# Kernel optimization log

Measured on AMD Instinct MI355X. Metric: run time of the kernel, lower is better.

The kernel has to match this reference:

```python
import jax, jax.numpy as jnp
import numpy as np

TOPK = 2


def _conv2d(x, w, b):
    # x: (B, Cin, H, W), w: (Cout, Cin, 3, 3), SAME padding (padding=1)
    y = jax.lax.conv_general_dilated(
        x, w, window_strides=(1, 1), padding='SAME',
        dimension_numbers=('NCHW', 'OIHW', 'NCHW'))
    return y + b[None, :, None, None]


def _msunit(x2d, c1w, c1b, c2w, c2b):
    # TimesNet-style 2D unit: conv(1->d_model) -> GELU -> conv(d_model->1)
    h = jax.nn.gelu(_conv2d(x2d, c1w, c1b))
    return _conv2d(h, c2w, c2b)


def setup_inputs():
    B, T, H, DM = 256, 2048, 720, 64
    key = jax.random.key(0)
    ks = jax.random.split(key, 5)
    x = jax.random.normal(ks[0], (B, 1, T), jnp.float32)
    conv1_w = jax.random.normal(ks[1], (DM, 1, 3, 3), jnp.float32) * 0.1
    conv1_b = jnp.zeros((DM,), jnp.float32)
    conv2_w = jax.random.normal(ks[2], (1, DM, 3, 3), jnp.float32) * 0.1
    conv2_b = jnp.zeros((1,), jnp.float32)
    head_w = jax.random.normal(ks[3], (H, T), jnp.float32) * 0.02
    head_b = jnp.zeros((H,), jnp.float32)
    return {'x': x, 'conv1_w': conv1_w, 'conv1_b': conv1_b,
            'conv2_w': conv2_w, 'conv2_b': conv2_b,
            'head_w': head_w, 'head_b': head_b}


def reference(x, conv1_w, conv1_b, conv2_w, conv2_b, head_w, head_b):
    B, _, T = x.shape
    # FFT amplitude spectrum, batch-averaged, drop DC bin
    amp = jnp.abs(jnp.fft.rfft(x[:, 0, :], axis=-1)).mean(0)[1:]
    vals, idx = jax.lax.top_k(amp, TOPK)
    # data-dependent period selection (mirrors .item() calls in torch -> Python ints)
    freqs = np.asarray(idx) + 1
    P_list = [max(1, int(round(T / int(f)))) for f in freqs]
    weights = jax.nn.softmax(vals.astype(x.dtype))
    y = jnp.zeros_like(x)
    for i, P in enumerate(P_list):
        cols = (T + P - 1) // P
        pad = P * cols - T
        xp = jnp.pad(x, ((0, 0), (0, 0), (0, pad)))
        x2d = xp.reshape(B, 1, cols, P).transpose(0, 1, 3, 2)  # (B,1,P,cols)
        y2d = _msunit(x2d, conv1_w, conv1_b, conv2_w, conv2_b)  # (B,1,P,cols)
        y1d = y2d.transpose(0, 1, 3, 2).reshape(B, 1, cols * P)[..., :T]
        y = y + weights[i] * y1d
    out = y[:, 0, :] @ head_w.T + head_b  # (B, horizon)
    return out
```

## Files before the change

### kernel.cpp

```cpp
#include <hip/hip_runtime.h>
#include <hip/hip_fp16.h>
#include <math.h>

#define T_LEN   2048
#define NB      256
#define N_FREQ  1024
#define DMODEL  64
#define HORIZON 720

#define WS_AMP  64
#define WS_Y0   2048
#define WS_Y1   (2048 + NB * T_LEN)

#define PMAX_FAST 191
#define CHUNK   1024
#define NCHUNK  2
#define HSTRIDE 1412
#define ZSLOT   1408
#define XS2N    1796
#define ZXS     1795

typedef _Float16 h4 __attribute__((ext_vector_type(4)));
typedef float    fx4 __attribute__((ext_vector_type(4)));

__device__ __forceinline__ float gelu_fast(float a) {
    float a2 = a * a;
    float z  = a * fmaf(-0.07135481627159498f, a2, -1.5957691216057308f);
    float e  = __expf(z);
    return a * __builtin_amdgcn_rcpf(1.0f + e);
}

__device__ __forceinline__ __half2 gelu2(float x, float y) {
    __half2 a  = __float22half2_rn(make_float2(x, y));
    __half2 a2 = __hmul2(a, a);
    const __half2 c2 = __float2half2_rn(-0.07135481627159498f);
    const __half2 c1 = __float2half2_rn(-1.5957691216057308f);
    __half2 z = __hmul2(a, __hfma2(c2, a2, c1));
    __half2 e = h2exp(z);
    const __half2 one = __float2half2_rn(1.0f);
    return __hmul2(a, h2rcp(__hadd2(one, e)));
}

__device__ __forceinline__ h4 gelu4(fx4 h) {
    union { __half2 p[2]; h4 v; } u;
    u.p[0] = gelu2(h[0], h[1]);
    u.p[1] = gelu2(h[2], h[3]);
    return u.v;
}

__device__ __forceinline__ float2 cmul(float2 a, float2 b) {
    return make_float2(a.x * b.x - a.y * b.y, a.x * b.y + a.y * b.x);
}

__device__ __forceinline__ unsigned magic_div(unsigned d) {
    return (unsigned)((0x100000000ULL + d - 1) / d);
}

__device__ __forceinline__ void compute_meta(const float* __restrict__ amp,
                                             float* sf, int* si, int tid,
                                             int& P1, int& cols1, int& P2, int& cols2,
                                             float& wg1, float& wg2) {
    float* v1s = sf;        float* v2s = sf + 256;
    int*   i1s = si;        int*   i2s = si + 256;
    float4 v4 = ((const float4*)amp)[tid];
    float vv[4] = {v4.x, v4.y, v4.z, v4.w};
    float v1 = -1e30f, v2 = -1e30f; int i1 = 1 << 30, i2 = 1 << 30;
    #pragma unroll
    for (int u = 0; u < 4; ++u) {
        int j = tid * 4 + u;
        float v = vv[u];
        if (v > v1) { v2 = v1; i2 = i1; v1 = v; i1 = j; }
        else if (v > v2) { v2 = v; i2 = j; }
    }
    v1s[tid] = v1; i1s[tid] = i1; v2s[tid] = v2; i2s[tid] = i2;
    __syncthreads();
    for (int st = 128; st > 0; st >>= 1) {
        if (tid < st) {
            float w1 = v1s[tid + st]; int j1 = i1s[tid + st];
            float w2 = v2s[tid + st]; int j2 = i2s[tid + st];
            float a1 = v1s[tid];      int a1i = i1s[tid];
            float a2 = v2s[tid];      int a2i = i2s[tid];
            float n1, n2; int n1i, n2i;
            bool w1_first = (w1 > a1) || (w1 == a1 && j1 < a1i);
            if (w1_first) {
                n1 = w1; n1i = j1;
                bool a1_next = (a1 > w2) || (a1 == w2 && a1i < j2);
                if (a1_next) { n2 = a1; n2i = a1i; } else { n2 = w2; n2i = j2; }
            } else {
                n1 = a1; n1i = a1i;
                bool w1_next = (w1 > a2) || (w1 == a2 && j1 < a2i);
                if (w1_next) { n2 = w1; n2i = j1; } else { n2 = a2; n2i = a2i; }
            }
            v1s[tid] = n1; i1s[tid] = n1i; v2s[tid] = n2; i2s[tid] = n2i;
        }
        __syncthreads();
    }
    float v1f = v1s[0], v2f = v2s[0];
    int f1 = i1s[0] + 1, f2 = i2s[0] + 1;
    __syncthreads();
    P1 = (int)llround(2048.0 / (double)f1); if (P1 < 1) P1 = 1;
    P2 = (int)llround(2048.0 / (double)f2); if (P2 < 1) P2 = 1;
    cols1 = (T_LEN + P1 - 1) / P1;
    cols2 = (T_LEN + P2 - 1) / P2;
    float mx = fmaxf(v1f, v2f);
    float e1 = __expf(v1f - mx), e2 = __expf(v2f - mx);
    float inv = 1.0f / (e1 + e2);
    wg1 = e1 * inv; wg2 = e2 * inv;
}

__global__ __launch_bounds__(256) void fft_amp_kernel(const float* __restrict__ x,
                                                      float* __restrict__ amp,
                                                      float* __restrict__ out) {
    __shared__ float2 buf0[1024];
    __shared__ float2 buf1[1024];
    __shared__ float2 tw[512];
    const int tid = threadIdx.x;
    const int b = blockIdx.x;

    if (tid < 180) {
        const int zi = b * 180 + tid;
        ((float4*)out)[zi] = make_float4(0.f, 0.f, 0.f, 0.f);
    }

    {
        float s, c;
        __sincosf((float)tid * 6.135923151542565e-3f, &s, &c);
        tw[tid] = make_float2(c, -s);
        __sincosf((float)(tid + 256) * 6.135923151542565e-3f, &s, &c);
        tw[tid + 256] = make_float2(c, -s);
    }
    const float2* xz = (const float2*)(x + b * T_LEN);
    buf0[tid]       = xz[tid];
    buf0[tid + 256] = xz[tid + 256];
    buf0[tid + 512] = xz[tid + 512];
    buf0[tid + 768] = xz[tid + 768];
    __syncthreads();

    float2* src = buf0;
    float2* dst = buf1;
    for (int s = 0; s < 10; s += 2) {
        const int Ns = 1 << s;
        const int j1 = tid;
        const int q  = j1 & (Ns - 1);
        const int hi = j1 >> s;
        float2 A = src[j1];
        float2 B = src[j1 + 512];
        float2 C = src[j1 + 256];
        float2 D = src[j1 + 768];
        float2 w  = tw[q << (9 - s)];
        float2 wB = cmul(w, B);
        float2 wD = cmul(w, D);
        float2 P0 = make_float2(A.x + wB.x, A.y + wB.y);
        float2 P1 = make_float2(A.x - wB.x, A.y - wB.y);
        float2 Q0 = make_float2(C.x + wD.x, C.y + wD.y);
        float2 Q1 = make_float2(C.x - wD.x, C.y - wD.y);
        float2 wa = tw[q << (8 - s)];
        float2 wb = tw[(q + Ns) << (8 - s)];
        float2 t0 = cmul(wa, Q0);
        float2 t1 = cmul(wb, Q1);
        const int O = (hi << (s + 2)) + q;
        dst[O]          = make_float2(P0.x + t0.x, P0.y + t0.y);
        dst[O + 2 * Ns] = make_float2(P0.x - t0.x, P0.y - t0.y);
        dst[O + Ns]     = make_float2(P1.x + t1.x, P1.y + t1.y);
        dst[O + 3 * Ns] = make_float2(P1.x - t1.x, P1.y - t1.y);
        __syncthreads();
        float2* tmp = src; src = dst; dst = tmp;
    }
    const int rot = (b * 8) & 1023;
    #pragma unroll
    for (int j = 0; j < 4; ++j) {
        const int kk = (tid + j * 256 + rot) & 1023;
        const int k  = kk + 1;
        float mag;
        if (k == 1024) {
            float2 Z0 = src[0];
            mag = fabsf(Z0.x - Z0.y) * (1.0f / 256.0f);
        } else {
            float2 Zk = src[k];
            float2 Zn = src[1024 - k];
            float Ax = 0.5f * (Zk.x + Zn.x), Ay = 0.5f * (Zk.y - Zn.y);
            float Bx = 0.5f * (Zk.y + Zn.y), By = -0.5f * (Zk.x - Zn.x);
            float sn, cs;
            __sincosf((float)k * 3.0679615757712823e-3f, &sn, &cs);
            float Xx = Ax + cs * Bx + sn * By;
            float Xy = Ay + cs * By - sn * Bx;
            mag = sqrtf(Xx * Xx + Xy * Xy) * (1.0f / 256.0f);
        }
        atomicAdd(amp + kk, mag);
    }
}

__global__ __launch_bounds__(256) void conv_fast_kernel(
    const float* __restrict__ x,
    const float* __restrict__ w1, const float* __restrict__ b1,
    const float* __restrict__ w2, const float* __restrict__ b2,
    const float* __restrict__ amp,
    float* __restrict__ ws)
{
    __shared__ __align__(16) _Float16 xs2[XS2N];
    __shared__ __align__(16) _Float16 dk[9][HSTRIDE];

    const int tid = threadIdx.x;
    const int b   = blockIdx.x >> 1;
    const int ci  = blockIdx.x & 1;
    const int t0  = ci * CHUNK;
    const int bT  = b * T_LEN;

    for (int j = tid; j < XS2N; j += 256) {
        const int t = t0 - 384 + j;
        xs2[j] = (_Float16)((j < 1792 && t >= 0 && t < T_LEN) ? x[bT + t] : 0.f);
    }

    int P1, cols1, P2, cols2; float wg1, wg2;
    compute_meta(amp, (float*)dk, (int*)dk + 512, tid, P1, cols1, P2, cols2, wg1, wg2);

    if (blockIdx.x == 0 && blockIdx.y == 0 && tid == 0) {
        int* mi = (int*)ws;
        mi[0] = P1; mi[1] = cols1; mi[2] = P2; mi[3] = cols2;
        ws[4] = wg1; ws[5] = wg2;
    }

    const int per  = blockIdx.y;
    const int P    = per == 0 ? P1 : P2;
    const int cols = per == 0 ? cols1 : cols2;
    if (P > PMAX_FAST || P < 2) return;
    const float wgt = per == 0 ? wg1 : wg2;
    float* yout = ws + (per == 0 ? WS_Y0 : WS_Y1);

    const int U0  = t0 - (P + 1);
    const int HN  = CHUNK + 2 * P + 2;
    const unsigned MP = magic_div((unsigned)P);
    const int IB0 = 383 - P;

    const int lane = tid & 63;
    const int wv   = tid >> 6;
    const int lm   = lane & 15;
    const int lg   = lane >> 4;

    h4  w1f[4], w2f[4];
    fx4 b1f[4];
    #pragma unroll
    for (int t = 0; t < 4; ++t) {
        #pragma unroll
        for (int i = 0; i < 4; ++i) {
            const int k = lg * 4 + i;
            w1f[t][i] = (_Float16)((k < 9) ? w1[(t * 16 + lm) * 9 + k] : 0.f);
            w2f[t][i] = (_Float16)((lm < 9) ? w2[(t * 16 + k) * 9 + lm] : 0.f);
            b1f[t][i] = b1[t * 16 + k];
        }
    }

    const int HN16 = (HN + 15) >> 4;
    const fx4 zf4 = {0.f, 0.f, 0.f, 0.f};

    for (int nt = wv; nt < HN16; nt += 4) {
        const int ih = nt * 16 + lm;
        const int u  = U0 + ih;
        const int uu = u < 0 ? 0 : u;
        const int cc = (int)__umulhi((unsigned)uu, MP);
        const int pp = uu - cc * P;
        const bool rm = pp > 0, rp = pp < P - 1, cm = cc > 0, cp = (cc + 1) < cols;
        const int ibase = ih + IB0;
        h4 xb;
        #pragma unroll
        for (int j = 0; j < 4; ++j) {
            const int tap = lg * 4 + j;
            const int q = (tap * 86) >> 8;
            const int r = tap - q * 3;
            const bool ok = (tap < 9)
                && (q > 0 || rm) && (q < 2 || rp)
                && (r > 0 || cm) && (r < 2 || cp);
            const int addr = ok ? (ibase + (r - 1) * P + (q - 1)) : ZXS;
            xb[j] = xs2[addr];
        }
        fx4 h0 = __builtin_amdgcn_mfma_f32_16x16x16f16(w1f[0], xb, b1f[0], 0, 0, 0);
        fx4 h1 = __builtin_amdgcn_mfma_f32_16x16x16f16(w1f[1], xb, b1f[1], 0, 0, 0);
        fx4 h2 = __builtin_amdgcn_mfma_f32_16x16x16f16(w1f[2], xb, b1f[2], 0, 0, 0);
        fx4 h3 = __builtin_amdgcn_mfma_f32_16x16x16f16(w1f[3], xb, b1f[3], 0, 0, 0);
        h4 g0 = gelu4(h0);
        h4 g1 = gelu4(h1);
        h4 g2 = gelu4(h2);
        h4 g3 = gelu4(h3);
        fx4 da = __builtin_amdgcn_mfma_f32_16x16x16f16(w2f[0], g0, zf4, 0, 0, 0);
        fx4 db = __builtin_amdgcn_mfma_f32_16x16x16f16(w2f[1], g1, zf4, 0, 0, 0);
        da = __builtin_amdgcn_mfma_f32_16x16x16f16(w2f[2], g2, da, 0, 0, 0);
        db = __builtin_amdgcn_mfma_f32_16x16x16f16(w2f[3], g3, db, 0, 0, 0);
        if (ih < HN) {
            #pragma unroll
            for (int i = 0; i < 4; ++i) {
                const int row = lg * 4 + i;
                if (row < 9) dk[row][ih] = (_Float16)(da[i] + db[i]);
            }
        }
    }
    if (tid < 9) dk[tid][ZSLOT] = (_Float16)0.f;
    __syncthreads();

    const float bias2 = b2[0];
    #pragma unroll
    for (int o = 0; o < 4; ++o) {
        const int t = t0 + tid + o * 256;
        const int iout = tid + o * 256 + (P + 1);
        const int cc = (int)__umulhi((unsigned)t, MP);
        const int pp = t - cc * P;
        const bool rm = pp > 0, rp = pp < P - 1, cm = cc > 0, cp = (cc + 1) < cols;
        const int i0 = (rm && cm) ? iout - P - 1 : ZSLOT;
        const int i1 = rm         ? iout - 1     : ZSLOT;
        const int i2 = (rm && cp) ? iout + P - 1 : ZSLOT;
        const int i3 = cm         ? iout - P     : ZSLOT;
        const int i5 = cp         ? iout + P     : ZSLOT;
        const int i6 = (rp && cm) ? iout - P + 1 : ZSLOT;
        const int i7 = rp         ? iout + 1     : ZSLOT;
        const int i8 = (rp && cp) ? iout + P + 1 : ZSLOT;
        float s = (float)dk[4][iout];
        s += (float)dk[0][i0]; s += (float)dk[1][i1]; s += (float)dk[2][i2];
        s += (float)dk[3][i3]; s += (float)dk[5][i5]; s += (float)dk[6][i6];
        s += (float)dk[7][i7]; s += (float)dk[8][i8];
        yout[bT + t] = wgt * (s + bias2);
    }
}

__global__ __launch_bounds__(256) void conv_unit_kernel(
    const float* __restrict__ x,
    const float* __restrict__ w1, const float* __restrict__ b1,
    const float* __restrict__ w2, const float* __restrict__ b2,
    float* __restrict__ ws)
{
    const int* mi = (const int*)ws;
    const int per   = blockIdx.y;
    const int P     = mi[per * 2 + 0];
    const int cols  = mi[per * 2 + 1];
    if (P <= PMAX_FAST && P >= 2) return;
    const float wgt = ws[4 + per];
    float* yout = ws + (per == 0 ? WS_Y0 : WS_Y1);

    __shared__ float w1s[DMODEL * 9];
    __shared__ float w2s[DMODEL * 9];
    __shared__ float b1s[DMODEL];
    __shared__ float xs[12][13];
    __shared__ float hs[DMODEL][101];

    const int tid = threadIdx.x;
    for (int i = tid; i < DMODEL * 9; i += 256) { w1s[i] = w1[i]; w2s[i] = w2[i]; }
    if (tid < DMODEL) b1s[tid] = b1[tid];
    const float bias2 = b2[0];

    const int tp = (P + 7) >> 3;
    const int tc = (cols + 7) >> 3;
    const int tiles_img = tp * tc;
    const int total = tiles_img * NB;

    for (int tile = blockIdx.x; tile < total; tile += gridDim.x) {
        const int b   = tile / tiles_img;
        const int ti  = tile - b * tiles_img;
        const int tpi = ti / tc;
        const int tci = ti - tpi * tc;
        const int p0 = tpi * 8, c0 = tci * 8;

        __syncthreads();
        if (tid < 144) {
            int i = tid / 12, j = tid - (tid / 12) * 12;
            int pp = p0 - 2 + i, cc = c0 - 2 + j;
            float v = 0.f;
            if (pp >= 0 && pp < P && cc >= 0 && cc < cols) {
                int t = cc * P + pp;
                if (t < T_LEN) v = x[b * T_LEN + t];
            }
            xs[i][j] = v;
        }
        __syncthreads();

        #pragma unroll
        for (int it = 0; it < 25; ++it) {
            int idx = it * 256 + tid;
            int ch = idx / 100;
            int px = idx - ch * 100;
            int pi = px / 10;
            int pj = px - pi * 10;
            const float* w = &w1s[ch * 9];
            float a = b1s[ch];
            a = fmaf(w[0], xs[pi    ][pj    ], a);
            a = fmaf(w[1], xs[pi    ][pj + 1], a);
            a = fmaf(w[2], xs[pi    ][pj + 2], a);
            a = fmaf(w[3], xs[pi + 1][pj    ], a);
            a = fmaf(w[4], xs[pi + 1][pj + 1], a);
            a = fmaf(w[5], xs[pi + 1][pj + 2], a);
            a = fmaf(w[6], xs[pi + 2][pj    ], a);
            a = fmaf(w[7], xs[pi + 2][pj + 1], a);
            a = fmaf(w[8], xs[pi + 2][pj + 2], a);
            float g = gelu_fast(a);
            int pp = p0 - 1 + pi, cc = c0 - 1 + pj;
            bool in_img = (pp >= 0) & (pp < P) & (cc >= 0) & (cc < cols);
            hs[ch][px] = in_img ? g : 0.0f;
        }
        __syncthreads();

        {
            const int pixel = tid >> 2, part = tid & 3;
            const int pi = pixel >> 3, pj = pixel & 7;
            const int base = pi * 10 + pj;
            float s = 0.f;
            for (int ch = part * 16; ch < part * 16 + 16; ++ch) {
                const float* w  = &w2s[ch * 9];
                const float* hr = &hs[ch][base];
                s = fmaf(w[0], hr[0],  s);
                s = fmaf(w[1], hr[1],  s);
                s = fmaf(w[2], hr[2],  s);
                s = fmaf(w[3], hr[10], s);
                s = fmaf(w[4], hr[11], s);
                s = fmaf(w[5], hr[12], s);
                s = fmaf(w[6], hr[20], s);
                s = fmaf(w[7], hr[21], s);
                s = fmaf(w[8], hr[22], s);
            }
            s += __shfl_down(s, 1);
            s += __shfl_down(s, 2);
            if (part == 0) {
                int pp = p0 + pi, cc = c0 + pj;
                if (pp < P && cc < cols) {
                    int t = cc * P + pp;
                    if (t < T_LEN) yout[b * T_LEN + t] = wgt * (s + bias2);
                }
            }
        }
    }
}

#define HG_KC 256
__global__ __launch_bounds__(256) void head_gemm_kernel(
    const float* __restrict__ ws, const float* __restrict__ hw,
    const float* __restrict__ hb, float* __restrict__ out)
{
    __shared__ _Float16 As[32][72];
    __shared__ _Float16 Bs[32][72];
    const float* y0 = ws + WS_Y0;
    const float* y1 = ws + WS_Y1;
    const int tid = threadIdx.x;
    const int b0 = blockIdx.x * 32, h0 = blockIdx.y * 32;
    const int kc0 = blockIdx.z * HG_KC;
    const int lane = tid & 63;
    const int wv   = tid >> 6;
    const int lm   = lane & 15;
    const int lg   = lane >> 4;
    const int wm   = (wv & 1) * 16;
    const int wn   = (wv >> 1) * 16;
    const int sr = tid >> 4;
    const int sq = (tid & 15) * 4;

    fx4 acc = {0.f, 0.f, 0.f, 0.f};

    for (int k0 = kc0; k0 < kc0 + HG_KC; k0 += 64) {
        #pragma unroll
        for (int hh = 0; hh < 2; ++hh) {
            const int r = sr + hh * 16;
            const int src = (b0 + r) * T_LEN + k0 + sq;
            float4 u = *(const float4*)(y0 + src);
            float4 v = *(const float4*)(y1 + src);
            As[r][sq + 0] = (_Float16)(u.x + v.x);
            As[r][sq + 1] = (_Float16)(u.y + v.y);
            As[r][sq + 2] = (_Float16)(u.z + v.z);
            As[r][sq + 3] = (_Float16)(u.w + v.w);
            const int hr = h0 + r;
            float4 w = (hr < HORIZON) ? *(const float4*)(hw + hr * T_LEN + k0 + sq)
                                      : make_float4(0.f, 0.f, 0.f, 0.f);
            Bs[r][sq + 0] = (_Float16)w.x;
            Bs[r][sq + 1] = (_Float16)w.y;
            Bs[r][sq + 2] = (_Float16)w.z;
            Bs[r][sq + 3] = (_Float16)w.w;
        }
        __syncthreads();
        #pragma unroll
        for (int kk = 0; kk < 64; kk += 16) {
            h4 af = *(const h4*)&As[wm + lm][kk + lg * 4];
            h4 bf = *(const h4*)&Bs[wn + lm][kk + lg * 4];
            acc = __builtin_amdgcn_mfma_f32_16x16x16f16(af, bf, acc, 0, 0, 0);
        }
        __syncthreads();
    }
    const int ncol = h0 + wn + lm;
    if (ncol < HORIZON) {
        const float bb = (blockIdx.z == 0) ? hb[ncol] : 0.f;
        #pragma unroll
        for (int i = 0; i < 4; ++i) {
            const int m = b0 + wm + lg * 4 + i;
            atomicAdd(&out[m * HORIZON + ncol], acc[i] + bb);
        }
    }
}

extern "C" void kernel_launch(void* const* d_in, const int* in_sizes, int n_in,
                              void* d_out, int out_size, void* d_ws, size_t ws_size,
                              hipStream_t stream) {
    const float* x   = (const float*)d_in[0];
    const float* c1w = (const float*)d_in[1];
    const float* c1b = (const float*)d_in[2];
    const float* c2w = (const float*)d_in[3];
    const float* c2b = (const float*)d_in[4];
    const float* hw  = (const float*)d_in[5];
    const float* hb  = (const float*)d_in[6];
    float* out = (float*)d_out;
    float* ws  = (float*)d_ws;

    float* amp = ws + WS_AMP;

    hipMemsetAsync(amp, 0, N_FREQ * sizeof(float), stream);
    fft_amp_kernel<<<NB, 256, 0, stream>>>(x, amp, out);
    conv_fast_kernel<<<dim3(NB * NCHUNK, 2), 256, 0, stream>>>(x, c1w, c1b, c2w, c2b, amp, ws);
    conv_unit_kernel<<<dim3(256, 2), 256, 0, stream>>>(x, c1w, c1b, c2w, c2b, ws);
    head_gemm_kernel<<<dim3(NB / 32, (HORIZON + 31) / 32, T_LEN / HG_KC), 256, 0, stream>>>(ws, hw, hb, out);
}
```

Measured before the change: 135.9 us.

## Fuse FFT, conv and head GEMM into one persistent kernel with grid barriers

Replaces the four separate launches (FFT amplitude, fast conv, fallback conv, head GEMM) with one 1024-block kernel that uses atomic-counter grid barriers between the phases. The goal is to remove per-launch overhead and inter-kernel gaps. It relies on all 1024 blocks being co-resident (launch bounds of 4 blocks per CU), and the spin barrier has a timeout break that could silently let blocks proceed. A barrier counter is zeroed by the memset each call.

```diff
diff --git a/kernel.cpp b/kernel.cpp
--- a/kernel.cpp
+++ b/kernel.cpp
@@ -8,17 +8,19 @@
 #define DMODEL  64
 #define HORIZON 720
 
+#define WS_BAR  8
 #define WS_AMP  64
 #define WS_Y0   2048
 #define WS_Y1   (2048 + NB * T_LEN)
 
 #define PMAX_FAST 191
 #define CHUNK   1024
-#define NCHUNK  2
 #define HSTRIDE 1412
 #define ZSLOT   1408
 #define XS2N    1796
 #define ZXS     1795
+
+#define SMEM_BYTES 31360
 
 typedef _Float16 h4 __attribute__((ext_vector_type(4)));
 typedef float    fx4 __attribute__((ext_vector_type(4)));
@@ -54,6 +56,21 @@
 
 __device__ __forceinline__ unsigned magic_div(unsigned d) {
     return (unsigned)((0x100000000ULL + d - 1) / d);
+}
+
+__device__ __forceinline__ void grid_barrier(unsigned* ctr, int tid) {
+    __syncthreads();
+    __threadfence();
+    if (tid == 0) {
+        __hip_atomic_fetch_add(ctr, 1u, __ATOMIC_ACQ_REL, __HIP_MEMORY_SCOPE_AGENT);
+        int spins = 0;
+        while (__hip_atomic_load(ctr, __ATOMIC_ACQUIRE, __HIP_MEMORY_SCOPE_AGENT) < 1024u) {
+            __builtin_amdgcn_s_sleep(8);
+            if (++spins > (1 << 22)) break;
+        }
+    }
+    __syncthreads();
+    __threadfence();
 }
 
 __device__ __forceinline__ void compute_meta(const float* __restrict__ amp,
@@ -108,382 +125,363 @@
     wg1 = e1 * inv; wg2 = e2 * inv;
 }
 
-__global__ __launch_bounds__(256) void fft_amp_kernel(const float* __restrict__ x,
-                                                      float* __restrict__ amp,
-                                                      float* __restrict__ out) {
-    __shared__ float2 buf0[1024];
-    __shared__ float2 buf1[1024];
-    __shared__ float2 tw[512];
-    const int tid = threadIdx.x;
-    const int b = blockIdx.x;
-
-    if (tid < 180) {
-        const int zi = b * 180 + tid;
-        ((float4*)out)[zi] = make_float4(0.f, 0.f, 0.f, 0.f);
-    }
-
-    {
-        float s, c;
-        __sincosf((float)tid * 6.135923151542565e-3f, &s, &c);
-        tw[tid] = make_float2(c, -s);
-        __sincosf((float)(tid + 256) * 6.135923151542565e-3f, &s, &c);
-        tw[tid + 256] = make_float2(c, -s);
-    }
-    const float2* xz = (const float2*)(x + b * T_LEN);
-    buf0[tid]       = xz[tid];
-    buf0[tid + 256] = xz[tid + 256];
-    buf0[tid + 512] = xz[tid + 512];
-    buf0[tid + 768] = xz[tid + 768];
-    __syncthreads();
-
-    float2* src = buf0;
-    float2* dst = buf1;
-    for (int s = 0; s < 10; s += 2) {
-        const int Ns = 1 << s;
-        const int j1 = tid;
-        const int q  = j1 & (Ns - 1);
-        const int hi = j1 >> s;
-        float2 A = src[j1];
-        float2 B = src[j1 + 512];
-        float2 C = src[j1 + 256];
-        float2 D = src[j1 + 768];
-        float2 w  = tw[q << (9 - s)];
-        float2 wB = cmul(w, B);
-        float2 wD = cmul(w, D);
-        float2 P0 = make_float2(A.x + wB.x, A.y + wB.y);
-        float2 P1 = make_float2(A.x - wB.x, A.y - wB.y);
-        float2 Q0 = make_float2(C.x + wD.x, C.y + wD.y);
-        float2 Q1 = make_float2(C.x - wD.x, C.y - wD.y);
-        float2 wa = tw[q << (8 - s)];
-        float2 wb = tw[(q + Ns) << (8 - s)];
-        float2 t0 = cmul(wa, Q0);
-        float2 t1 = cmul(wb, Q1);
-        const int O = (hi << (s + 2)) + q;
-        dst[O]          = make_float2(P0.x + t0.x, P0.y + t0.y);
-        dst[O + 2 * Ns] = make_float2(P0.x - t0.x, P0.y - t0.y);
-        dst[O + Ns]     = make_float2(P1.x + t1.x, P1.y + t1.y);
-        dst[O + 3 * Ns] = make_float2(P1.x - t1.x, P1.y - t1.y);
-        __syncthreads();
-        float2* tmp = src; src = dst; dst = tmp;
-    }
-    const int rot = (b * 8) & 1023;
-    #pragma unroll
-    for (int j = 0; j < 4; ++j) {
-        const int kk = (tid + j * 256 + rot) & 1023;
-        const int k  = kk + 1;
-        float mag;
-        if (k == 1024) {
-            float2 Z0 = src[0];
-            mag = fabsf(Z0.x - Z0.y) * (1.0f / 256.0f);
-        } else {
-            float2 Zk = src[k];
-            float2 Zn = src[1024 - k];
-            float Ax = 0.5f * (Zk.x + Zn.x), Ay = 0.5f * (Zk.y - Zn.y);
-            float Bx = 0.5f * (Zk.y + Zn.y), By = -0.5f * (Zk.x - Zn.x);
-            float sn, cs;
-            __sincosf((float)k * 3.0679615757712823e-3f, &sn, &cs);
-            float Xx = Ax + cs * Bx + sn * By;
-            float Xy = Ay + cs * By - sn * Bx;
-            mag = sqrtf(Xx * Xx + Xy * Xy) * (1.0f / 256.0f);
-        }
-        atomicAdd(amp + kk, mag);
-    }
-}
-
-__global__ __launch_bounds__(256) void conv_fast_kernel(
+__global__ __launch_bounds__(256, 4) void mega_kernel(
     const float* __restrict__ x,
     const float* __restrict__ w1, const float* __restrict__ b1,
     const float* __restrict__ w2, const float* __restrict__ b2,
-    const float* __restrict__ amp,
-    float* __restrict__ ws)
+    const float* __restrict__ hw, const float* __restrict__ hb,
+    float* __restrict__ ws, float* __restrict__ out)
 {
-    __shared__ __align__(16) _Float16 xs2[XS2N];
-    __shared__ __align__(16) _Float16 dk[9][HSTRIDE];
-
+    __shared__ __align__(16) unsigned char smem[SMEM_BYTES];
     const int tid = threadIdx.x;
-    const int b   = blockIdx.x >> 1;
-    const int ci  = blockIdx.x & 1;
-    const int t0  = ci * CHUNK;
-    const int bT  = b * T_LEN;
-
-    for (int j = tid; j < XS2N; j += 256) {
-        const int t = t0 - 384 + j;
-        xs2[j] = (_Float16)((j < 1792 && t >= 0 && t < T_LEN) ? x[bT + t] : 0.f);
-    }
-
-    int P1, cols1, P2, cols2; float wg1, wg2;
-    compute_meta(amp, (float*)dk, (int*)dk + 512, tid, P1, cols1, P2, cols2, wg1, wg2);
-
-    if (blockIdx.x == 0 && blockIdx.y == 0 && tid == 0) {
-        int* mi = (int*)ws;
-        mi[0] = P1; mi[1] = cols1; mi[2] = P2; mi[3] = cols2;
-        ws[4] = wg1; ws[5] = wg2;
-    }
-
-    const int per  = blockIdx.y;
-    const int P    = per == 0 ? P1 : P2;
-    const int cols = per == 0 ? cols1 : cols2;
-    if (P > PMAX_FAST || P < 2) return;
-    const float wgt = per == 0 ? wg1 : wg2;
-    float* yout = ws + (per == 0 ? WS_Y0 : WS_Y1);
-
-    const int U0  = t0 - (P + 1);
-    const int HN  = CHUNK + 2 * P + 2;
-    const unsigned MP = magic_div((unsigned)P);
-    const int IB0 = 383 - P;
-
-    const int lane = tid & 63;
-    const int wv   = tid >> 6;
-    const int lm   = lane & 15;
-    const int lg   = lane >> 4;
-
-    h4  w1f[4], w2f[4];
-    fx4 b1f[4];
-    #pragma unroll
-    for (int t = 0; t < 4; ++t) {
-        #pragma unroll
-        for (int i = 0; i < 4; ++i) {
-            const int k = lg * 4 + i;
-            w1f[t][i] = (_Float16)((k < 9) ? w1[(t * 16 + lm) * 9 + k] : 0.f);
-            w2f[t][i] = (_Float16)((lm < 9) ? w2[(t * 16 + k) * 9 + lm] : 0.f);
-            b1f[t][i] = b1[t * 16 + k];
-        }
-    }
-
-    const int HN16 = (HN + 15) >> 4;
-    const fx4 zf4 = {0.f, 0.f, 0.f, 0.f};
-
-    for (int nt = wv; nt < HN16; nt += 4) {
-        const int ih = nt * 16 + lm;
-        const int u  = U0 + ih;
-        const int uu = u < 0 ? 0 : u;
-        const int cc = (int)__umulhi((unsigned)uu, MP);
-        const int pp = uu - cc * P;
-        const bool rm = pp > 0, rp = pp < P - 1, cm = cc > 0, cp = (cc + 1) < cols;
-        const int ibase = ih + IB0;
-        h4 xb;
+    const int bid = blockIdx.x;
+    float* amp = ws + WS_AMP;
+    unsigned* bar = (unsigned*)ws + WS_BAR;
+
+    if (tid < 45) ((float4*)out)[bid * 45 + tid] = make_float4(0.f, 0.f, 0.f, 0.f);
+
+    if (bid < NB) {
+        float2* buf0 = (float2*)smem;
+        float2* buf1 = (float2*)(smem + 8192);
+        float2* tw   = (float2*)(smem + 16384);
+        const int b = bid;
+        {
+            float s, c;
+            __sincosf((float)tid * 6.135923151542565e-3f, &s, &c);
+            tw[tid] = make_float2(c, -s);
+            __sincosf((float)(tid + 256) * 6.135923151542565e-3f, &s, &c);
+            tw[tid + 256] = make_float2(c, -s);
+        }
+        const float2* xz = (const float2*)(x + b * T_LEN);
+        buf0[tid]       = xz[tid];
+        buf0[tid + 256] = xz[tid + 256];
+        buf0[tid + 512] = xz[tid + 512];
+        buf0[tid + 768] = xz[tid + 768];
+        __syncthreads();
+
+        float2* src = buf0;
+        float2* dst = buf1;
+        for (int s = 0; s < 10; s += 2) {
+            const int Ns = 1 << s;
+            const int j1 = tid;
+            const int q  = j1 & (Ns - 1);
+            const int hi = j1 >> s;
+            float2 A = src[j1];
+            float2 B = src[j1 + 512];
+            float2 C = src[j1 + 256];
+            float2 D = src[j1 + 768];
+            float2 w  = tw[q << (9 - s)];
+            float2 wB = cmul(w, B);
+            float2 wD = cmul(w, D);
+            float2 P0v = make_float2(A.x + wB.x, A.y + wB.y);
+            float2 P1v = make_float2(A.x - wB.x, A.y - wB.y);
+            float2 Q0 = make_float2(C.x + wD.x, C.y + wD.y);
+            float2 Q1 = make_float2(C.x - wD.x, C.y - wD.y);
+            float2 wa = tw[q << (8 - s)];
+            float2 wb = tw[(q + Ns) << (8 - s)];
+            float2 t0 = cmul(wa, Q0);
+            float2 t1 = cmul(wb, Q1);
+            const int O = (hi << (s + 2)) + q;
+            dst[O]          = make_float2(P0v.x + t0.x, P0v.y + t0.y);
+            dst[O + 2 * Ns] = make_float2(P0v.x - t0.x, P0v.y - t0.y);
+            dst[O + Ns]     = make_float2(P1v.x + t1.x, P1v.y + t1.y);
+            dst[O + 3 * Ns] = make_float2(P1v.x - t1.x, P1v.y - t1.y);
+            __syncthreads();
+            float2* tmp = src; src = dst; dst = tmp;
+        }
+        const int rot = (b * 8) & 1023;
         #pragma unroll
         for (int j = 0; j < 4; ++j) {
-            const int tap = lg * 4 + j;
-            const int q = (tap * 86) >> 8;
-            const int r = tap - q * 3;
-            const bool ok = (tap < 9)
-                && (q > 0 || rm) && (q < 2 || rp)
-                && (r > 0 || cm) && (r < 2 || cp);
-            const int addr = ok ? (ibase + (r - 1) * P + (q - 1)) : ZXS;
-            xb[j] = xs2[addr];
-        }
-        fx4 h0 = __builtin_amdgcn_mfma_f32_16x16x16f16(w1f[0], xb, b1f[0], 0, 0, 0);
-        fx4 h1 = __builtin_amdgcn_mfma_f32_16x16x16f16(w1f[1], xb, b1f[1], 0, 0, 0);
-        fx4 h2 = __builtin_amdgcn_mfma_f32_16x16x16f16(w1f[2], xb, b1f[2], 0, 0, 0);
-        fx4 h3 = __builtin_amdgcn_mfma_f32_16x16x16f16(w1f[3], xb, b1f[3], 0, 0, 0);
-        h4 g0 = gelu4(h0);
-        h4 g1 = gelu4(h1);
-        h4 g2 = gelu4(h2);
-        h4 g3 = gelu4(h3);
-        fx4 da = __builtin_amdgcn_mfma_f32_16x16x16f16(w2f[0], g0, zf4, 0, 0, 0);
-        fx4 db = __builtin_amdgcn_mfma_f32_16x16x16f16(w2f[1], g1, zf4, 0, 0, 0);
-        da = __builtin_amdgcn_mfma_f32_16x16x16f16(w2f[2], g2, da, 0, 0, 0);
-        db = __builtin_amdgcn_mfma_f32_16x16x16f16(w2f[3], g3, db, 0, 0, 0);
-        if (ih < HN) {
+            const int kk = (tid + j * 256 + rot) & 1023;
+            const int k  = kk + 1;
+            float mag;
+            if (k == 1024) {
+                float2 Z0 = src[0];
+                mag = fabsf(Z0.x - Z0.y) * (1.0f / 256.0f);
+            } else {
+                float2 Zk = src[k];
+                float2 Zn = src[1024 - k];
+                float Ax = 0.5f * (Zk.x + Zn.x), Ay = 0.5f * (Zk.y - Zn.y);
+                float Bx = 0.5f * (Zk.y + Zn.y), By = -0.5f * (Zk.x - Zn.x);
+                float sn, cs;
+                __sincosf((float)k * 3.0679615757712823e-3f, &sn, &cs);
+                float Xx = Ax + cs * Bx + sn * By;
+                float Xy = Ay + cs * By - sn * Bx;
+                mag = sqrtf(Xx * Xx + Xy * Xy) * (1.0f / 256.0f);
+            }
+            atomicAdd(amp + kk, mag);
+        }
+    }
+
+    grid_barrier(&bar[0], tid);
+
+    {
+        _Float16 (*dk)[HSTRIDE] = (_Float16 (*)[HSTRIDE])smem;
+        _Float16* xs2 = (_Float16*)(smem + 25424);
+
+        const int per = bid >> 9;
+        const int u   = bid & 511;
+        const int b   = u >> 1;
+        const int ci  = u & 1;
+        const int t0  = ci * CHUNK;
+        const int bT  = b * T_LEN;
+
+        for (int j = tid; j < XS2N; j += 256) {
+            const int t = t0 - 384 + j;
+            xs2[j] = (_Float16)((j < 1792 && t >= 0 && t < T_LEN) ? x[bT + t] : 0.f);
+        }
+
+        int P1_, cols1, P2_, cols2; float wg1, wg2;
+        compute_meta(amp, (float*)dk, (int*)dk + 512, tid, P1_, cols1, P2_, cols2, wg1, wg2);
+
+        const int P    = per == 0 ? P1_ : P2_;
+        const int cols = per == 0 ? cols1 : cols2;
+        const float wgt = per == 0 ? wg1 : wg2;
+        float* yout = ws + (per == 0 ? WS_Y0 : WS_Y1);
+
+        if (P >= 2 && P <= PMAX_FAST) {
+            const int U0  = t0 - (P + 1);
+            const int HN  = CHUNK + 2 * P + 2;
+            const unsigned MP = magic_div((unsigned)P);
+            const int IB0 = 383 - P;
+
+            const int lane = tid & 63;
+            const int wv   = tid >> 6;
+            const int lm   = lane & 15;
+            const int lg   = lane >> 4;
+
+            h4  w1f[4], w2f[4];
+            fx4 b1f[4];
+            #pragma unroll
+            for (int t = 0; t < 4; ++t) {
+                #pragma unroll
+                for (int i = 0; i < 4; ++i) {
+                    const int k = lg * 4 + i;
+                    w1f[t][i] = (_Float16)((k < 9) ? w1[(t * 16 + lm) * 9 + k] : 0.f);
+                    w2f[t][i] = (_Float16)((lm < 9) ? w2[(t * 16 + k) * 9 + lm] : 0.f);
+                    b1f[t][i] = b1[t * 16 + k];
+                }
+            }
+
+            const int HN16 = (HN + 15) >> 4;
+            const fx4 zf4 = {0.f, 0.f, 0.f, 0.f};
+
+            for (int nt = wv; nt < HN16; nt += 4) {
+                const int ih = nt * 16 + lm;
+                const int uu0 = U0 + ih;
+                const int uu = uu0 < 0 ? 0 : uu0;
+                const int cc = (int)__umulhi((unsigned)uu, MP);
+                const int pp = uu - cc * P;
+                const bool rm = pp > 0, rp = pp < P - 1, cm = cc > 0, cp = (cc + 1) < cols;
+                const int ibase = ih + IB0;
+                h4 xb;
+                #pragma unroll
+                for (int j = 0; j < 4; ++j) {
+                    const int tap = lg * 4 + j;
+                    const int q = (tap * 86) >> 8;
+                    const int r = tap - q * 3;
+                    const bool ok = (tap < 9)
+                        && (q > 0 || rm) && (q < 2 || rp)
+                        && (r > 0 || cm) && (r < 2 || cp);
+                    const int addr = ok ? (ibase + (r - 1) * P + (q - 1)) : ZXS;
+                    xb[j] = xs2[addr];
+                }
+                fx4 h0 = __builtin_amdgcn_mfma_f32_16x16x16f16(w1f[0], xb, b1f[0], 0, 0, 0);
+                fx4 h1 = __builtin_amdgcn_mfma_f32_16x16x16f16(w1f[1], xb, b1f[1], 0, 0, 0);
+                fx4 h2 = __builtin_amdgcn_mfma_f32_16x16x16f16(w1f[2], xb, b1f[2], 0, 0, 0);
+                fx4 h3 = __builtin_amdgcn_mfma_f32_16x16x16f16(w1f[3], xb, b1f[3], 0, 0, 0);
+                h4 g0 = gelu4(h0);
+                h4 g1 = gelu4(h1);
+                h4 g2 = gelu4(h2);
+                h4 g3 = gelu4(h3);
+                fx4 da = __builtin_amdgcn_mfma_f32_16x16x16f16(w2f[0], g0, zf4, 0, 0, 0);
+                fx4 db = __builtin_amdgcn_mfma_f32_16x16x16f16(w2f[1], g1, zf4, 0, 0, 0);
+                da = __builtin_amdgcn_mfma_f32_16x16x16f16(w2f[2], g2, da, 0, 0, 0);
+                db = __builtin_amdgcn_mfma_f32_16x16x16f16(w2f[3], g3, db, 0, 0, 0);
+                if (ih < HN) {
+                    #pragma unroll
+                    for (int i = 0; i < 4; ++i) {
+                        const int row = lg * 4 + i;
+                        if (row < 9) dk[row][ih] = (_Float16)(da[i] + db[i]);
+                    }
+                }
+            }
+            if (tid < 9) dk[tid][ZSLOT] = (_Float16)0.f;
+            __syncthreads();
+
+            const float bias2 = b2[0];
+            #pragma unroll
+            for (int o = 0; o < 4; ++o) {
+                const int t = t0 + tid + o * 256;
+                const int iout = tid + o * 256 + (P + 1);
+                const int cc = (int)__umulhi((unsigned)t, MP);
+                const int pp = t - cc * P;
+                const bool rm = pp > 0, rp = pp < P - 1, cm = cc > 0, cp = (cc + 1) < cols;
+                const int i0 = (rm && cm) ? iout - P - 1 : ZSLOT;
+                const int i1 = rm         ? iout - 1     : ZSLOT;
+                const int i2 = (rm && cp) ? iout + P - 1 : ZSLOT;
+                const int i3 = cm         ? iout - P     : ZSLOT;
+                const int i5 = cp         ? iout + P     : ZSLOT;
+                const int i6 = (rp && cm) ? iout - P + 1 : ZSLOT;
+                const int i7 = rp         ? iout + 1     : ZSLOT;
+                const int i8 = (rp && cp) ? iout + P + 1 : ZSLOT;
+                float s = (float)dk[4][iout];
+                s += (float)dk[0][i0]; s += (float)dk[1][i1]; s += (float)dk[2][i2];
+                s += (float)dk[3][i3]; s += (float)dk[5][i5]; s += (float)dk[6][i6];
+                s += (float)dk[7][i7]; s += (float)dk[8][i8];
+                yout[bT + t] = wgt * (s + bias2);
+            }
+        } else {
+            float* w1s = (float*)smem;
+            float* w2s = w1s + 576;
+            float* b1s = w2s + 576;
+            float (*fxs)[13] = (float (*)[13])(b1s + 64);
+            float (*hs)[101] = (float (*)[101])(b1s + 64 + 156);
+
+            for (int i = tid; i < DMODEL * 9; i += 256) { w1s[i] = w1[i]; w2s[i] = w2[i]; }
+            if (tid < DMODEL) b1s[tid] = b1[tid];
+            const float bias2 = b2[0];
+
+            const int tp = (P + 7) >> 3;
+            const int tc = (cols + 7) >> 3;
+            const int tiles_img = tp * tc;
+            const int total = tiles_img * NB;
+
+            for (int tile = u; tile < total; tile += 512) {
+                const int bb = tile / tiles_img;
+                const int ti  = tile - bb * tiles_img;
+                const int tpi = ti / tc;
+                const int tci = ti - tpi * tc;
+                const int p0 = tpi * 8, c0 = tci * 8;
+
+                __syncthreads();
+                if (tid < 144) {
+                    int i = tid / 12, j = tid - (tid / 12) * 12;
+                    int pp = p0 - 2 + i, cc = c0 - 2 + j;
+                    float v = 0.f;
+                    if (pp >= 0 && pp < P && cc >= 0 && cc < cols) {
+                        int t = cc * P + pp;
+                        if (t < T_LEN) v = x[bb * T_LEN + t];
+                    }
+                    fxs[i][j] = v;
+                }
+                __syncthreads();
+
+                for (int it = 0; it < 25; ++it) {
+                    int idx = it * 256 + tid;
+                    int ch = idx / 100;
+                    int px = idx - ch * 100;
+                    int pi = px / 10;
+                    int pj = px - pi * 10;
+                    const float* w = &w1s[ch * 9];
+                    float a = b1s[ch];
+                    a = fmaf(w[0], fxs[pi    ][pj    ], a);
+                    a = fmaf(w[1], fxs[pi    ][pj + 1], a);
+                    a = fmaf(w[2], fxs[pi    ][pj + 2], a);
+                    a = fmaf(w[3], fxs[pi + 1][pj    ], a);
+                    a = fmaf(w[4], fxs[pi + 1][pj + 1], a);
+                    a = fmaf(w[5], fxs[pi + 1][pj + 2], a);
+                    a = fmaf(w[6], fxs[pi + 2][pj    ], a);
+                    a = fmaf(w[7], fxs[pi + 2][pj + 1], a);
+                    a = fmaf(w[8], fxs[pi + 2][pj + 2], a);
+                    float g = gelu_fast(a);
+                    int pp = p0 - 1 + pi, cc = c0 - 1 + pj;
+                    bool in_img = (pp >= 0) & (pp < P) & (cc >= 0) & (cc < cols);
+                    hs[ch][px] = in_img ? g : 0.0f;
+                }
+                __syncthreads();
+
+                {
+                    const int pixel = tid >> 2, part = tid & 3;
+                    const int pi = pixel >> 3, pj = pixel & 7;
+                    const int base = pi * 10 + pj;
+                    float s = 0.f;
+                    for (int ch = part * 16; ch < part * 16 + 16; ++ch) {
+                        const float* w  = &w2s[ch * 9];
+                        const float* hr = &hs[ch][base];
+                        s = fmaf(w[0], hr[0],  s);
+                        s = fmaf(w[1], hr[1],  s);
+                        s = fmaf(w[2], hr[2],  s);
+                        s = fmaf(w[3], hr[10], s);
+                        s = fmaf(w[4], hr[11], s);
+                        s = fmaf(w[5], hr[12], s);
+                        s = fmaf(w[6], hr[20], s);
+                        s = fmaf(w[7], hr[21], s);
+                        s = fmaf(w[8], hr[22], s);
+                    }
+                    s += __shfl_down(s, 1);
+                    s += __shfl_down(s, 2);
+                    if (part == 0) {
+                        int pp = p0 + pi, cc = c0 + pj;
+                        if (pp < P && cc < cols) {
+                            int t = cc * P + pp;
+                            if (t < T_LEN) yout[bb * T_LEN + t] = wgt * (s + bias2);
+                        }
+                    }
+                }
+            }
+        }
+    }
+
+    grid_barrier(&bar[1], tid);
+
+    if (bid < 736) {
+        _Float16 (*As)[72] = (_Float16 (*)[72])smem;
+        _Float16 (*Bs)[72] = (_Float16 (*)[72])(smem + 4608);
+        const float* y0 = ws + WS_Y0;
+        const float* y1 = ws + WS_Y1;
+        const int kz = bid & 3;
+        const int tl = bid >> 2;
+        const int b0 = (tl & 7) * 32;
+        const int h0 = (tl >> 3) * 32;
+        const int kc0 = kz * 512;
+        const int lane = tid & 63;
+        const int wv   = tid >> 6;
+        const int lm   = lane & 15;
+        const int lg   = lane >> 4;
+        const int wm   = (wv & 1) * 16;
+        const int wn   = (wv >> 1) * 16;
+        const int sr = tid >> 4;
+        const int sq = (tid & 15) * 4;
+
+        fx4 acc = {0.f, 0.f, 0.f, 0.f};
+
+        for (int k0 = kc0; k0 < kc0 + 512; k0 += 64) {
+            #pragma unroll
+            for (int hh = 0; hh < 2; ++hh) {
+                const int r = sr + hh * 16;
+                const int src = (b0 + r) * T_LEN + k0 + sq;
+                float4 uu = *(const float4*)(y0 + src);
+                float4 vv = *(const float4*)(y1 + src);
+                As[r][sq + 0] = (_Float16)(uu.x + vv.x);
+                As[r][sq + 1] = (_Float16)(uu.y + vv.y);
+                As[r][sq + 2] = (_Float16)(uu.z + vv.z);
+                As[r][sq + 3] = (_Float16)(uu.w + vv.w);
+                const int hr = h0 + r;
+                float4 w = (hr < HORIZON) ? *(const float4*)(hw + hr * T_LEN + k0 + sq)
+                                          : make_float4(0.f, 0.f, 0.f, 0.f);
+                Bs[r][sq + 0] = (_Float16)w.x;
+                Bs[r][sq + 1] = (_Float16)w.y;
+                Bs[r][sq + 2] = (_Float16)w.z;
+                Bs[r][sq + 3] = (_Float16)w.w;
+            }
+            __syncthreads();
+            #pragma unroll
+            for (int kk = 0; kk < 64; kk += 16) {
+                h4 af = *(const h4*)&As[wm + lm][kk + lg * 4];
+                h4 bf = *(const h4*)&Bs[wn + lm][kk + lg * 4];
+                acc = __builtin_amdgcn_mfma_f32_16x16x16f16(af, bf, acc, 0, 0, 0);
+            }
+            __syncthreads();
+        }
+        const int ncol = h0 + wn + lm;
+        if (ncol < HORIZON) {
+            const float bb = (kz == 0) ? hb[ncol] : 0.f;
             #pragma unroll
             for (int i = 0; i < 4; ++i) {
-                const int row = lg * 4 + i;
-                if (row < 9) dk[row][ih] = (_Float16)(da[i] + db[i]);
-            }
-        }
-    }
-    if (tid < 9) dk[tid][ZSLOT] = (_Float16)0.f;
-    __syncthreads();
-
-    const float bias2 = b2[0];
-    #pragma unroll
-    for (int o = 0; o < 4; ++o) {
-        const int t = t0 + tid + o * 256;
-        const int iout = tid + o * 256 + (P + 1);
-        const int cc = (int)__umulhi((unsigned)t, MP);
-        const int pp = t - cc * P;
-        const bool rm = pp > 0, rp = pp < P - 1, cm = cc > 0, cp = (cc + 1) < cols;
-        const int i0 = (rm && cm) ? iout - P - 1 : ZSLOT;
-        const int i1 = rm         ? iout - 1     : ZSLOT;
-        const int i2 = (rm && cp) ? iout + P - 1 : ZSLOT;
-        const int i3 = cm         ? iout - P     : ZSLOT;
-        const int i5 = cp         ? iout + P     : ZSLOT;
-        const int i6 = (rp && cm) ? iout - P + 1 : ZSLOT;
-        const int i7 = rp         ? iout + 1     : ZSLOT;
-        const int i8 = (rp && cp) ? iout + P + 1 : ZSLOT;
-        float s = (float)dk[4][iout];
-        s += (float)dk[0][i0]; s += (float)dk[1][i1]; s += (float)dk[2][i2];
-        s += (float)dk[3][i3]; s += (float)dk[5][i5]; s += (float)dk[6][i6];
-        s += (float)dk[7][i7]; s += (float)dk[8][i8];
-        yout[bT + t] = wgt * (s + bias2);
-    }
-}
-
-__global__ __launch_bounds__(256) void conv_unit_kernel(
-    const float* __restrict__ x,
-    const float* __restrict__ w1, const float* __restrict__ b1,
-    const float* __restrict__ w2, const float* __restrict__ b2,
-    float* __restrict__ ws)
-{
-    const int* mi = (const int*)ws;
-    const int per   = blockIdx.y;
-    const int P     = mi[per * 2 + 0];
-    const int cols  = mi[per * 2 + 1];
-    if (P <= PMAX_FAST && P >= 2) return;
-    const float wgt = ws[4 + per];
-    float* yout = ws + (per == 0 ? WS_Y0 : WS_Y1);
-
-    __shared__ float w1s[DMODEL * 9];
-    __shared__ float w2s[DMODEL * 9];
-    __shared__ float b1s[DMODEL];
-    __shared__ float xs[12][13];
-    __shared__ float hs[DMODEL][101];
-
-    const int tid = threadIdx.x;
-    for (int i = tid; i < DMODEL * 9; i += 256) { w1s[i] = w1[i]; w2s[i] = w2[i]; }
-    if (tid < DMODEL) b1s[tid] = b1[tid];
-    const float bias2 = b2[0];
-
-    const int tp = (P + 7) >> 3;
-    const int tc = (cols + 7) >> 3;
-    const int tiles_img = tp * tc;
-    const int total = tiles_img * NB;
-
-    for (int tile = blockIdx.x; tile < total; tile += gridDim.x) {
-        const int b   = tile / tiles_img;
-        const int ti  = tile - b * tiles_img;
-        const int tpi = ti / tc;
-        const int tci = ti - tpi * tc;
-        const int p0 = tpi * 8, c0 = tci * 8;
-
-        __syncthreads();
-        if (tid < 144) {
-            int i = tid / 12, j = tid - (tid / 12) * 12;
-            int pp = p0 - 2 + i, cc = c0 - 2 + j;
-            float v = 0.f;
-            if (pp >= 0 && pp < P && cc >= 0 && cc < cols) {
-                int t = cc * P + pp;
-                if (t < T_LEN) v = x[b * T_LEN + t];
-            }
-            xs[i][j] = v;
-        }
-        __syncthreads();
-
-        #pragma unroll
-        for (int it = 0; it < 25; ++it) {
-            int idx = it * 256 + tid;
-            int ch = idx / 100;
-            int px = idx - ch * 100;
-            int pi = px / 10;
-            int pj = px - pi * 10;
-            const float* w = &w1s[ch * 9];
-            float a = b1s[ch];
-            a = fmaf(w[0], xs[pi    ][pj    ], a);
-            a = fmaf(w[1], xs[pi    ][pj + 1], a);
-            a = fmaf(w[2], xs[pi    ][pj + 2], a);
-            a = fmaf(w[3], xs[pi + 1][pj    ], a);
-            a = fmaf(w[4], xs[pi + 1][pj + 1], a);
-            a = fmaf(w[5], xs[pi + 1][pj + 2], a);
-            a = fmaf(w[6], xs[pi + 2][pj    ], a);
-            a = fmaf(w[7], xs[pi + 2][pj + 1], a);
-            a = fmaf(w[8], xs[pi + 2][pj + 2], a);
-            float g = gelu_fast(a);
-            int pp = p0 - 1 + pi, cc = c0 - 1 + pj;
-            bool in_img = (pp >= 0) & (pp < P) & (cc >= 0) & (cc < cols);
-            hs[ch][px] = in_img ? g : 0.0f;
-        }
-        __syncthreads();
-
-        {
-            const int pixel = tid >> 2, part = tid & 3;
-            const int pi = pixel >> 3, pj = pixel & 7;
-            const int base = pi * 10 + pj;
-            float s = 0.f;
-            for (int ch = part * 16; ch < part * 16 + 16; ++ch) {
-                const float* w  = &w2s[ch * 9];
-                const float* hr = &hs[ch][base];
-                s = fmaf(w[0], hr[0],  s);
-                s = fmaf(w[1], hr[1],  s);
-                s = fmaf(w[2], hr[2],  s);
-                s = fmaf(w[3], hr[10], s);
-                s = fmaf(w[4], hr[11], s);
-                s = fmaf(w[5], hr[12], s);
-                s = fmaf(w[6], hr[20], s);
-                s = fmaf(w[7], hr[21], s);
-                s = fmaf(w[8], hr[22], s);
-            }
-            s += __shfl_down(s, 1);
-            s += __shfl_down(s, 2);
-            if (part == 0) {
-                int pp = p0 + pi, cc = c0 + pj;
-                if (pp < P && cc < cols) {
-                    int t = cc * P + pp;
-                    if (t < T_LEN) yout[b * T_LEN + t] = wgt * (s + bias2);
-                }
-            }
-        }
-    }
-}
-
-#define HG_KC 256
-__global__ __launch_bounds__(256) void head_gemm_kernel(
-    const float* __restrict__ ws, const float* __restrict__ hw,
-    const float* __restrict__ hb, float* __restrict__ out)
-{
-    __shared__ _Float16 As[32][72];
-    __shared__ _Float16 Bs[32][72];
-    const float* y0 = ws + WS_Y0;
-    const float* y1 = ws + WS_Y1;
-    const int tid = threadIdx.x;
-    const int b0 = blockIdx.x * 32, h0 = blockIdx.y * 32;
-    const int kc0 = blockIdx.z * HG_KC;
-    const int lane = tid & 63;
-    const int wv   = tid >> 6;
-    const int lm   = lane & 15;
-    const int lg   = lane >> 4;
-    const int wm   = (wv & 1) * 16;
-    const int wn   = (wv >> 1) * 16;
-    const int sr = tid >> 4;
-    const int sq = (tid & 15) * 4;
-
-    fx4 acc = {0.f, 0.f, 0.f, 0.f};
-
-    for (int k0 = kc0; k0 < kc0 + HG_KC; k0 += 64) {
-        #pragma unroll
-        for (int hh = 0; hh < 2; ++hh) {
-            const int r = sr + hh * 16;
-            const int src = (b0 + r) * T_LEN + k0 + sq;
-            float4 u = *(const float4*)(y0 + src);
-            float4 v = *(const float4*)(y1 + src);
-            As[r][sq + 0] = (_Float16)(u.x + v.x);
-            As[r][sq + 1] = (_Float16)(u.y + v.y);
-            As[r][sq + 2] = (_Float16)(u.z + v.z);
-            As[r][sq + 3] = (_Float16)(u.w + v.w);
-            const int hr = h0 + r;
-            float4 w = (hr < HORIZON) ? *(const float4*)(hw + hr * T_LEN + k0 + sq)
-                                      : make_float4(0.f, 0.f, 0.f, 0.f);
-            Bs[r][sq + 0] = (_Float16)w.x;
-            Bs[r][sq + 1] = (_Float16)w.y;
-            Bs[r][sq + 2] = (_Float16)w.z;
-            Bs[r][sq + 3] = (_Float16)w.w;
-        }
-        __syncthreads();
-        #pragma unroll
-        for (int kk = 0; kk < 64; kk += 16) {
-            h4 af = *(const h4*)&As[wm + lm][kk + lg * 4];
-            h4 bf = *(const h4*)&Bs[wn + lm][kk + lg * 4];
-            acc = __builtin_amdgcn_mfma_f32_16x16x16f16(af, bf, acc, 0, 0, 0);
-        }
-        __syncthreads();
-    }
-    const int ncol = h0 + wn + lm;
-    if (ncol < HORIZON) {
-        const float bb = (blockIdx.z == 0) ? hb[ncol] : 0.f;
-        #pragma unroll
-        for (int i = 0; i < 4; ++i) {
-            const int m = b0 + wm + lg * 4 + i;
-            atomicAdd(&out[m * HORIZON + ncol], acc[i] + bb);
+                const int m = b0 + wm + lg * 4 + i;
+                atomicAdd(&out[m * HORIZON + ncol], acc[i] + bb);
+            }
         }
     }
 }
@@ -501,11 +499,6 @@
     float* out = (float*)d_out;
     float* ws  = (float*)d_ws;
 
-    float* amp = ws + WS_AMP;
-
-    hipMemsetAsync(amp, 0, N_FREQ * sizeof(float), stream);
-    fft_amp_kernel<<<NB, 256, 0, stream>>>(x, amp, out);
-    conv_fast_kernel<<<dim3(NB * NCHUNK, 2), 256, 0, stream>>>(x, c1w, c1b, c2w, c2b, amp, ws);
-    conv_unit_kernel<<<dim3(256, 2), 256, 0, stream>>>(x, c1w, c1b, c2w, c2b, ws);
-    head_gemm_kernel<<<dim3(NB / 32, (HORIZON + 31) / 32, T_LEN / HG_KC), 256, 0, stream>>>(ws, hw, hb, out);
-}
+    hipMemsetAsync(ws, 0, (64 + N_FREQ) * sizeof(float), stream);
+    mega_kernel<<<1024, 256, 0, stream>>>(x, c1w, c1b, c2w, c2b, hw, hb, ws, out);
+}
```

Result: slower. 413.8 us (+204.5%).
